# Kernel tuning notes

Measured on AMD Instinct MI355X. Metric: run time of the kernel, lower is better.

The kernel has to match this reference:

```python
import jax, jax.numpy as jnp
import numpy as np

W = 128      # window_size
BACK = 1     # look_backward
FWD = 0      # look_forward (causal)


def _look_around(x, backward=BACK, forward=FWD, pad_value=-1):
    t = x.shape[1]
    pads = [(0, 0), (backward, forward)] + [(0, 0)] * (x.ndim - 2)
    p = jnp.pad(x, pads, constant_values=pad_value)
    return jnp.concatenate([p[:, i:i + t] for i in range(forward + backward + 1)], axis=2)


def setup_inputs() -> dict:
    key = jax.random.key(0)
    kq, kk, kv = jax.random.split(key, 3)
    B, H, T, D = 4, 8, 8192, 64
    q = jax.random.normal(kq, (B, H, T, D), jnp.float32)
    k = jax.random.normal(kk, (B, H, T, D), jnp.float32)
    v = jax.random.normal(kv, (B, H, T, D), jnp.float32)
    return {"q": q, "k": k, "v": v}


def reference(q, k, v):
    B, H, T, D = q.shape
    win = T // W
    # flatten batch/head, split into windows
    bq = q.reshape(B * H, win, W, D)
    bk = k.reshape(B * H, win, W, D)
    bv = v.reshape(B * H, win, W, D)
    bk = _look_around(bk)
    bv = _look_around(bv)

    bq_t = jnp.arange(T, dtype=jnp.int32).reshape(1, win, W)       # query positions
    bq_k = _look_around(bq_t, pad_value=-1)                        # key positions (pad = -1)

    scale = D ** -0.5
    dots = jnp.einsum('bwid,bwjd->bwij', bq, bk) * scale
    mask_value = -jnp.finfo(dots.dtype).max

    causal_mask = bq_t[:, :, :, None] < bq_k[:, :, None, :]
    pad_mask = (bq_k == -1)[:, :, None, :]
    dots = jnp.where(causal_mask | pad_mask, mask_value, dots)

    attn = jax.nn.softmax(dots, axis=-1)
    out = jnp.einsum('bwij,bwjd->bwid', attn, bv)
    return out.reshape(B, H, T, D)
```

## Files before the change

kernel.cpp:

```cpp
#include <hip/hip_runtime.h>
#include <hip/hip_bf16.h>

typedef __bf16 bf16x8 __attribute__((ext_vector_type(8)));
typedef float  f32x4  __attribute__((ext_vector_type(4)));
typedef float  f32x16 __attribute__((ext_vector_type(16)));
typedef unsigned int u32x4 __attribute__((ext_vector_type(4)));

#define TQ 8192
#define DD 64
#define PSTRV 264

static __device__ __forceinline__ unsigned pack2_bf16(float lo, float hi) {
    unsigned short a = __builtin_bit_cast(unsigned short, (__bf16)lo);
    unsigned short b = __builtin_bit_cast(unsigned short, (__bf16)hi);
    return ((unsigned)b << 16) | (unsigned)a;
}

__global__ __launch_bounds__(256, 4)
void lattn_kernel(const float* __restrict__ q, const float* __restrict__ k,
                  const float* __restrict__ v, float* __restrict__ out)
{
    __shared__ __align__(16) unsigned char smem[DD * PSTRV * 2];
    __bf16* Vt = (__bf16*)smem;
    float*  Ot = (float*)smem;

    const int bx   = blockIdx.x;
    const int bh   = bx >> 6;
    const int w    = bx & 63;
    const int tid  = threadIdx.x;
    const int lane = tid & 63;
    const int wv   = tid >> 6;
    const int l31  = lane & 31;
    const int hi   = lane >> 5;

    const size_t base  = ((size_t)bh * TQ + w * 128) * DD;
    const int    krow0 = w * 128 - 128;

    bf16x8 qf[4];
    {
        const float* qp = q + base + (size_t)(wv * 32 + l31) * DD + hi * 8;
        #pragma unroll
        for (int s = 0; s < 4; ++s) {
            f32x4 a = *(const f32x4*)(qp + 16 * s);
            f32x4 b = *(const f32x4*)(qp + 16 * s + 4);
            #pragma unroll
            for (int e = 0; e < 4; ++e) { qf[s][e] = (__bf16)a[e]; qf[s][4 + e] = (__bf16)b[e]; }
        }
    }

    #pragma unroll
    for (int it = 0; it < 16; ++it) {
        int flat = it * 256 + tid;
        int j  = flat >> 4;
        int d0 = (flat & 15) * 4;
        int gr = krow0 + j;
        f32x4 val = {0.f, 0.f, 0.f, 0.f};
        if (gr >= 0) val = *(const f32x4*)(v + ((size_t)bh * TQ + gr) * DD + d0);
        #pragma unroll
        for (int c = 0; c < 4; ++c) Vt[(d0 + c) * PSTRV + j] = (__bf16)val[c];
    }
    __syncthreads();

    f32x16 o0 = {}, o1 = {};
    float m2 = -3.0e38f, lsum = 0.f;
    const float C = 0.18033688011112042f;

    const int kb0   = (w == 0) ? 4 : 0;
    const int kbend = wv + 4;
    for (int kb = kb0; kb <= kbend; ++kb) {
        f32x16 sacc = {};
        {
            const float* kp = k + ((size_t)bh * TQ + (krow0 + kb * 32 + l31)) * DD + hi * 8;
            #pragma unroll
            for (int s = 0; s < 4; ++s) {
                f32x4 a = *(const f32x4*)(kp + 16 * s);
                f32x4 b = *(const f32x4*)(kp + 16 * s + 4);
                bf16x8 kf;
                #pragma unroll
                for (int e = 0; e < 4; ++e) { kf[e] = (__bf16)a[e]; kf[4 + e] = (__bf16)b[e]; }
                sacc = __builtin_amdgcn_mfma_f32_32x32x16_bf16(kf, qf[s], sacc, 0, 0, 0);
            }
        }
        float p[16];
        float locmax = -3.0e38f;
        const bool partial = (kb == kbend);
        #pragma unroll
        for (int r = 0; r < 16; ++r) {
            float sv = sacc[r] * C;
            int j = (r & 3) + 8 * (r >> 2) + 4 * hi;
            if (partial && (j > l31)) sv = -3.0e38f;
            p[r] = sv;
            locmax = fmaxf(locmax, sv);
        }
        locmax = fmaxf(locmax, __shfl_xor(locmax, 32, 64));
        float mnew = fmaxf(m2, locmax);
        float fac  = exp2f(m2 - mnew);
        float ts = 0.f;
        #pragma unroll
        for (int r = 0; r < 16; ++r) { float e = exp2f(p[r] - mnew); p[r] = e; ts += e; }
        ts += __shfl_xor(ts, 32, 64);
        lsum = lsum * fac + ts;
        m2 = mnew;
        #pragma unroll
        for (int r = 0; r < 16; ++r) { o0[r] *= fac; o1[r] *= fac; }

        unsigned pk[8], xw[8];
        #pragma unroll
        for (int m = 0; m < 8; ++m) pk[m] = pack2_bf16(p[2 * m], p[2 * m + 1]);
        #pragma unroll
        for (int m = 0; m < 8; ++m) xw[m] = (unsigned)__shfl_xor((int)pk[m], 32, 64);
        u32x4 f0, f1;
        f0[0] = hi ? xw[2] : pk[0]; f0[1] = hi ? xw[3] : pk[1];
        f0[2] = hi ? pk[2] : xw[0]; f0[3] = hi ? pk[3] : xw[1];
        f1[0] = hi ? xw[6] : pk[4]; f1[1] = hi ? xw[7] : pk[5];
        f1[2] = hi ? pk[6] : xw[4]; f1[3] = hi ? pk[7] : xw[5];
        bf16x8 pf0 = __builtin_bit_cast(bf16x8, f0);
        bf16x8 pf1 = __builtin_bit_cast(bf16x8, f1);

        const __bf16* vb = &Vt[l31 * PSTRV + kb * 32 + hi * 8];
        bf16x8 v00 = *(const bf16x8*)(vb);
        bf16x8 v01 = *(const bf16x8*)(vb + 16);
        bf16x8 v10 = *(const bf16x8*)(vb + 32 * PSTRV);
        bf16x8 v11 = *(const bf16x8*)(vb + 32 * PSTRV + 16);
        o0 = __builtin_amdgcn_mfma_f32_32x32x16_bf16(v00, pf0, o0, 0, 0, 0);
        o0 = __builtin_amdgcn_mfma_f32_32x32x16_bf16(v01, pf1, o0, 0, 0, 0);
        o1 = __builtin_amdgcn_mfma_f32_32x32x16_bf16(v10, pf0, o1, 0, 0, 0);
        o1 = __builtin_amdgcn_mfma_f32_32x32x16_bf16(v11, pf1, o1, 0, 0, 0);
    }

    float rl = 1.0f / lsum;
    __syncthreads();
    {
        int iq = wv * 32 + l31;
        #pragma unroll
        for (int r = 0; r < 16; ++r) {
            int d = (r & 3) + 8 * (r >> 2) + 4 * hi;
            Ot[d * 132 + iq]        = o0[r] * rl;
            Ot[(d + 32) * 132 + iq] = o1[r] * rl;
        }
    }
    __syncthreads();
    {
        int iq = tid >> 1;
        int dh = (tid & 1) * 32;
        float* op = out + base + (size_t)iq * DD + dh;
        #pragma unroll
        for (int u = 0; u < 8; ++u) {
            f32x4 val;
            #pragma unroll
            for (int c = 0; c < 4; ++c) val[c] = Ot[(dh + u * 4 + c) * 132 + iq];
            *(f32x4*)(op + u * 4) = val;
        }
    }
}

extern "C" void kernel_launch(void* const* d_in, const int* in_sizes, int n_in,
                              void* d_out, int out_size, void* d_ws, size_t ws_size,
                              hipStream_t stream) {
    const float* q = (const float*)d_in[0];
    const float* k = (const float*)d_in[1];
    const float* v = (const float*)d_in[2];
    float* out = (float*)d_out;
    dim3 grid(32 * 64);
    dim3 block(256);
    lattn_kernel<<<grid, block, 0, stream>>>(q, k, v, out);
}
```

Before: 90.01 us.

## Prefetch next K block, swizzle V smem, remap blocks, raise MFMA priority

Loads of the next K tile are software-pipelined into registers during the current block's softmax and PV MMAs, so global latency is no longer exposed before each QK MFMA chain. The transposed V tile in shared memory is XOR-swizzled to cut bank conflicts on the transposed writes and reads. Block indices are remapped so consecutive workgroups land on different head/window groups, possibly to spread work across XCDs. s_setprio is raised around the MFMA sequences. Together these raise register pressure under the 4-waves launch bound.

New measurement: 84.16 us. 1.07x faster.

```diff
diff --git a/kernel.cpp b/kernel.cpp
--- a/kernel.cpp
+++ b/kernel.cpp
@@ -14,6 +14,10 @@
     unsigned short a = __builtin_bit_cast(unsigned short, (__bf16)lo);
     unsigned short b = __builtin_bit_cast(unsigned short, (__bf16)hi);
     return ((unsigned)b << 16) | (unsigned)a;
+}
+
+static __device__ __forceinline__ int vt_idx(int d, int j) {
+    return d * PSTRV + ((((j >> 3) ^ ((d >> 2) & 7)) << 3) | (j & 7));
 }
 
 __global__ __launch_bounds__(256, 4)
@@ -24,7 +28,8 @@
     __bf16* Vt = (__bf16*)smem;
     float*  Ot = (float*)smem;
 
-    const int bx   = blockIdx.x;
+    const int bx0  = blockIdx.x;
+    const int bx   = ((bx0 & 7) << 8) | (bx0 >> 3);
     const int bh   = bx >> 6;
     const int w    = bx & 63;
     const int tid  = threadIdx.x;
@@ -35,6 +40,20 @@
 
     const size_t base  = ((size_t)bh * TQ + w * 128) * DD;
     const int    krow0 = w * 128 - 128;
+
+    const int kb0   = (w == 0) ? 4 : 0;
+    const int kbend = wv + 4;
+
+    const float* kbase = k + ((size_t)bh * TQ + krow0) * DD + hi * 8;
+    f32x4 kn[8];
+    {
+        const float* kp = kbase + (size_t)(kb0 * 32 + l31) * DD;
+        #pragma unroll
+        for (int s = 0; s < 4; ++s) {
+            kn[2 * s]     = *(const f32x4*)(kp + 16 * s);
+            kn[2 * s + 1] = *(const f32x4*)(kp + 16 * s + 4);
+        }
+    }
 
     bf16x8 qf[4];
     {
@@ -57,7 +76,14 @@
         f32x4 val = {0.f, 0.f, 0.f, 0.f};
         if (gr >= 0) val = *(const f32x4*)(v + ((size_t)bh * TQ + gr) * DD + d0);
         #pragma unroll
-        for (int c = 0; c < 4; ++c) Vt[(d0 + c) * PSTRV + j] = (__bf16)val[c];
+        for (int c = 0; c < 4; ++c) Vt[vt_idx(d0 + c, j)] = (__bf16)val[c];
+    }
+
+    bf16x8 kf[4];
+    #pragma unroll
+    for (int s = 0; s < 4; ++s) {
+        #pragma unroll
+        for (int e = 0; e < 4; ++e) { kf[s][e] = (__bf16)kn[2 * s][e]; kf[s][4 + e] = (__bf16)kn[2 * s + 1][e]; }
     }
     __syncthreads();
 
@@ -65,22 +91,23 @@
     float m2 = -3.0e38f, lsum = 0.f;
     const float C = 0.18033688011112042f;
 
-    const int kb0   = (w == 0) ? 4 : 0;
-    const int kbend = wv + 4;
     for (int kb = kb0; kb <= kbend; ++kb) {
+        if (kb < kbend) {
+            const float* kp = kbase + (size_t)((kb + 1) * 32 + l31) * DD;
+            #pragma unroll
+            for (int s = 0; s < 4; ++s) {
+                kn[2 * s]     = *(const f32x4*)(kp + 16 * s);
+                kn[2 * s + 1] = *(const f32x4*)(kp + 16 * s + 4);
+            }
+        }
+
         f32x16 sacc = {};
-        {
-            const float* kp = k + ((size_t)bh * TQ + (krow0 + kb * 32 + l31)) * DD + hi * 8;
-            #pragma unroll
-            for (int s = 0; s < 4; ++s) {
-                f32x4 a = *(const f32x4*)(kp + 16 * s);
-                f32x4 b = *(const f32x4*)(kp + 16 * s + 4);
-                bf16x8 kf;
-                #pragma unroll
-                for (int e = 0; e < 4; ++e) { kf[e] = (__bf16)a[e]; kf[4 + e] = (__bf16)b[e]; }
-                sacc = __builtin_amdgcn_mfma_f32_32x32x16_bf16(kf, qf[s], sacc, 0, 0, 0);
-            }
-        }
+        __builtin_amdgcn_s_setprio(1);
+        #pragma unroll
+        for (int s = 0; s < 4; ++s)
+            sacc = __builtin_amdgcn_mfma_f32_32x32x16_bf16(kf[s], qf[s], sacc, 0, 0, 0);
+        __builtin_amdgcn_s_setprio(0);
+
         float p[16];
         float locmax = -3.0e38f;
         const bool partial = (kb == kbend);
@@ -117,15 +144,23 @@
         bf16x8 pf0 = __builtin_bit_cast(bf16x8, f0);
         bf16x8 pf1 = __builtin_bit_cast(bf16x8, f1);
 
-        const __bf16* vb = &Vt[l31 * PSTRV + kb * 32 + hi * 8];
-        bf16x8 v00 = *(const bf16x8*)(vb);
-        bf16x8 v01 = *(const bf16x8*)(vb + 16);
-        bf16x8 v10 = *(const bf16x8*)(vb + 32 * PSTRV);
-        bf16x8 v11 = *(const bf16x8*)(vb + 32 * PSTRV + 16);
+        const int jb = kb * 32 + hi * 8;
+        bf16x8 v00 = *(const bf16x8*)&Vt[vt_idx(l31,      jb)];
+        bf16x8 v01 = *(const bf16x8*)&Vt[vt_idx(l31,      jb + 16)];
+        bf16x8 v10 = *(const bf16x8*)&Vt[vt_idx(l31 + 32, jb)];
+        bf16x8 v11 = *(const bf16x8*)&Vt[vt_idx(l31 + 32, jb + 16)];
+        __builtin_amdgcn_s_setprio(1);
         o0 = __builtin_amdgcn_mfma_f32_32x32x16_bf16(v00, pf0, o0, 0, 0, 0);
         o0 = __builtin_amdgcn_mfma_f32_32x32x16_bf16(v01, pf1, o0, 0, 0, 0);
         o1 = __builtin_amdgcn_mfma_f32_32x32x16_bf16(v10, pf0, o1, 0, 0, 0);
         o1 = __builtin_amdgcn_mfma_f32_32x32x16_bf16(v11, pf1, o1, 0, 0, 0);
+        __builtin_amdgcn_s_setprio(0);
+
+        #pragma unroll
+        for (int s = 0; s < 4; ++s) {
+            #pragma unroll
+            for (int e = 0; e < 4; ++e) { kf[s][e] = (__bf16)kn[2 * s][e]; kf[s][4 + e] = (__bf16)kn[2 * s + 1][e]; }
+        }
     }
 
     float rl = 1.0f / lsum;
```
